# Performance work log

Hardware: AMD Instinct MI355X
Metric: run time of the kernel (lower is better)

Reference implementation:

```python
import jax, jax.numpy as jnp
import numpy as np

B, NN, D = 16, 50, 400
H, DH = 20, 20
ATT_H = 128
NEWS = 20000
K = 10
STEPS, SLOTS = 6, 10
EPS = 1e-5


def _layer_norm(x, g, b):
    m = jnp.mean(x, -1, keepdims=True)
    v = jnp.mean(jnp.square(x - m), -1, keepdims=True)
    return (x - m) * jax.lax.rsqrt(v + EPS) * g + b


def setup_inputs():
    key = jax.random.key(0)
    ks = jax.random.split(key, 9)
    s = 1.0 / np.sqrt(D)
    return {
        "news_input": jax.random.normal(ks[0], (B, NN, D), jnp.float32),
        "outputs_table": jax.random.normal(ks[1], (NEWS, K, D), jnp.float32) * 0.1,
        "Wq": jax.random.normal(ks[2], (D, H * DH), jnp.float32) * s,
        "Wk": jax.random.normal(ks[3], (D, H * DH), jnp.float32) * s,
        "Wv": jax.random.normal(ks[4], (D, H * DH), jnp.float32) * s,
        "ln1_g": jnp.ones((D,), jnp.float32),
        "ln1_b": jnp.zeros((D,), jnp.float32),
        "fc1_w": jax.random.normal(ks[5], (D, ATT_H), jnp.float32) * s,
        "fc1_b": jnp.zeros((ATT_H,), jnp.float32),
        "fc2_w": jax.random.normal(ks[6], (ATT_H, 1), jnp.float32) * (1.0 / np.sqrt(ATT_H)),
        "fc2_b": jnp.zeros((1,), jnp.float32),
        "ln2_g": jnp.ones((D,), jnp.float32),
        "ln2_b": jnp.zeros((D,), jnp.float32),
        "click_history": jax.random.randint(ks[7], (B, NN), 1, NEWS + 1),
        "neighbor_table": jax.random.randint(ks[8], (NEWS + 1, K), 1, NEWS + 1),
        "mask": jnp.ones((B, 50 * SLOTS), jnp.int32),
    }


def _traverse(news_input, outputs_table, click_history, neighbor_table):
    # Vectorized form of the per-item 6-hop neighbor traversal.
    def step(carry, _):
        idx, dead = carry                                          # [B,N] int, [B,N] bool
        vg = outputs_table[idx - 1]                                # [B,N,K,D] gather
        scores = jnp.einsum('bnkd,bnd->bnk', vg, news_input)      # [B,N,K]
        mx_i = jnp.argmax(scores, -1)
        mx_v = jnp.take_along_axis(scores, mx_i[..., None], -1)[..., 0]
        nz = scores != 0
        any_nz = jnp.any(nz, -1)
        nz_i = jnp.argmax(jnp.where(nz, scores, -jnp.inf), -1)
        hop = (mx_v == 0) & jnp.logical_not(dead)                  # max score exactly 0 -> follow graph
        sel_i = jnp.where(hop & any_nz, nz_i, mx_i)
        new_dead = dead | (hop & jnp.logical_not(any_nz))
        nbr = jnp.take_along_axis(neighbor_table[idx], sel_i[..., None], -1)[..., 0]
        new_idx = jnp.where(hop & any_nz, nbr, idx)
        sel = jnp.take_along_axis(vg, sel_i[..., None, None], 2)[..., 0, :]
        sel = jnp.where(new_dead[..., None], 0.0, sel)
        return (new_idx, new_dead), sel

    init = (click_history, jnp.zeros(click_history.shape, bool))
    _, sels = jax.lax.scan(step, init, None, length=STEPS)         # [6,B,N,D]
    sels = jnp.moveaxis(sels, 0, 2)                                # [B,N,6,D]
    valid = jnp.any(news_input != 0, -1).astype(sels.dtype)        # skip all-zero news rows
    sels = sels * valid[..., None, None]
    res = jnp.pad(sels, ((0, 0), (0, 0), (0, SLOTS - STEPS), (0, 0)))
    if NN < 50:
        res = jnp.pad(res, ((0, 0), (0, 50 - NN), (0, 0), (0, 0)))
    return res                                                      # [B,50,10,D]


def _mha(x, mask, Wq, Wk, Wv):
    L = x.shape[1]
    q = (x @ Wq).reshape(-1, L, H, DH).transpose(0, 2, 1, 3)
    k = (x @ Wk).reshape(-1, L, H, DH).transpose(0, 2, 1, 3)
    v = (x @ Wv).reshape(-1, L, H, DH).transpose(0, 2, 1, 3)
    sc = jnp.einsum('bhqd,bhkd->bhqk', q, k) / np.float32(np.sqrt(DH))
    sc = jnp.where(mask[:, None, None, :] > 0, sc, -1e9)
    a = jax.nn.softmax(sc, -1)
    o = jnp.einsum('bhqk,bhkd->bhqd', a, v)
    return o.transpose(0, 2, 1, 3).reshape(-1, L, H * DH)


def _att_pool(x, mask, fc1_w, fc1_b, fc2_w, fc2_b):
    e = jnp.tanh(x @ fc1_w + fc1_b) @ fc2_w + fc2_b                # [B*50,10,1]
    e = jnp.where(mask[..., None] > 0, e, -1e9)
    a = jax.nn.softmax(e, 1)
    return jnp.sum(a * x, 1)


def reference(news_input, outputs_table, Wq, Wk, Wv, ln1_g, ln1_b,
              fc1_w, fc1_b, fc2_w, fc2_b, ln2_g, ln2_b,
              click_history, neighbor_table, mask):
    res = _traverse(news_input, outputs_table, click_history, neighbor_table)
    x = res.reshape(-1, 50 * SLOTS, D)
    x = _mha(x, mask, Wq, Wk, Wv)
    x = x.reshape(-1, SLOTS, D)
    x = _layer_norm(x, ln1_g, ln1_b)
    x = _att_pool(x, mask.reshape(-1, SLOTS), fc1_w, fc1_b, fc2_w, fc2_b)
    x = _layer_norm(x, ln2_g, ln2_b)
    return x.reshape(-1, 50, D)
```

## Files before the change

### kernel.cpp

```cpp
#include <hip/hip_runtime.h>
#include <hip/hip_bf16.h>
#include <math.h>

#define B 16
#define NN 50
#define D 400
#define H 20
#define DH 20
#define ATT_H 128
#define NEWS 20000
#define K 10
#define STEPS 6
#define SLOTS 10
#define L 500
#define EPS 1e-5f

#define XP 416
#define NC 1200

typedef short short8 __attribute__((ext_vector_type(8)));
typedef float floatx4 __attribute__((ext_vector_type(4)));

__device__ __forceinline__ short f2bf(float f) {
    __hip_bfloat16 h = __float2bfloat16(f);
    return *reinterpret_cast<short*>(&h);
}

__global__ __launch_bounds__(256) void k_traverse(
    const float* __restrict__ news,
    const float* __restrict__ table,
    const int*   __restrict__ click,
    const int*   __restrict__ nbrt,
    short* __restrict__ x)
{
    __shared__ float ssc[K];

    int item = blockIdx.x;
    int b = item / NN, n = item % NN;
    int tid = threadIdx.x;
    int lane = tid & 63, w = tid >> 6;

    float nv[7];
    bool nzf = false;
    #pragma unroll
    for (int i = 0; i < 7; i++) {
        int d = lane + 64 * i;
        float v = (d < D) ? news[(size_t)item * D + d] : 0.0f;
        nv[i] = v;
        nzf |= (v != 0.0f);
    }
    float valid = __any(nzf) ? 1.0f : 0.0f;

    int idx = click[item];
    bool dead = false;
    short* xbase = x + (size_t)(b * L + n * SLOTS) * XP;

    for (int step = 0; step < STEPS; step++) {
        const float* tb = table + (size_t)(idx - 1) * K * D;
        for (int kk = w; kk < K; kk += 4) {
            float p = 0.0f;
            #pragma unroll
            for (int i = 0; i < 7; i++) {
                int d = lane + 64 * i;
                if (d < D) p += tb[kk * D + d] * nv[i];
            }
            #pragma unroll
            for (int off = 32; off > 0; off >>= 1) p += __shfl_xor(p, off);
            if (lane == 0) ssc[kk] = p;
        }
        __syncthreads();

        float scores[K];
        #pragma unroll
        for (int kk = 0; kk < K; kk++) scores[kk] = ssc[kk];

        int mx_i = 0; float mx_v = scores[0];
        #pragma unroll
        for (int kk = 1; kk < K; kk++)
            if (scores[kk] > mx_v) { mx_v = scores[kk]; mx_i = kk; }

        bool any_nz = false; int nz_i = 0; float nz_v = -INFINITY;
        #pragma unroll
        for (int kk = 0; kk < K; kk++) {
            if (scores[kk] != 0.0f) {
                if (!any_nz || scores[kk] > nz_v) { nz_v = scores[kk]; nz_i = kk; }
                any_nz = true;
            }
        }

        bool hop = (mx_v == 0.0f) && !dead;
        int sel_i = (hop && any_nz) ? nz_i : mx_i;
        bool new_dead = dead || (hop && !any_nz);
        int nbr = nbrt[(size_t)idx * K + sel_i];
        int new_idx = (hop && any_nz) ? nbr : idx;

        float scale = new_dead ? 0.0f : valid;
        const float* selrow = tb + (size_t)sel_i * D;
        short* xr = xbase + (size_t)step * XP;
        for (int d = tid; d < XP; d += 256)
            xr[d] = (d < D) ? f2bf(selrow[d] * scale) : (short)0;

        idx = new_idx; dead = new_dead;
        __syncthreads();
    }
    for (int s = STEPS; s < SLOTS; s++) {
        short* xr = xbase + (size_t)s * XP;
        for (int d = tid; d < XP; d += 256) xr[d] = 0;
    }
}

__global__ __launch_bounds__(256) void k_wconvT(
    const float* __restrict__ Wq, const float* __restrict__ Wk,
    const float* __restrict__ Wv, short* __restrict__ wT)
{
    int c = blockIdx.x;
    int z = c / 400, n = c % 400;
    const float* W = (z == 0) ? Wq : (z == 1) ? Wk : Wv;
    for (int k = threadIdx.x; k < XP; k += 256)
        wT[(size_t)c * XP + k] = (k < 400) ? f2bf(W[(size_t)k * 400 + n]) : (short)0;
}

#define BM 128
#define BN 64
#define BKK 32

__global__ __launch_bounds__(256) void k_qkv_mfma(
    const short* __restrict__ xg,
    const short* __restrict__ wT,
    float* __restrict__ c)
{
    __shared__ short xs[BM][BKK + 8];
    __shared__ short wt[BN][BKK + 8];

    int tid = threadIdx.x;
    int m0 = blockIdx.x * BM;
    int n0 = blockIdx.y * BN;
    int lane = tid & 63, w = tid >> 6;
    int wr = w >> 1, wc = w & 1;
    int quad = lane >> 4, l16 = lane & 15;

    floatx4 acc[4][2];
    #pragma unroll
    for (int i = 0; i < 4; i++)
        #pragma unroll
        for (int j = 0; j < 2; j++) acc[i][j] = (floatx4){0.f, 0.f, 0.f, 0.f};

    int xr = tid >> 1, xc = (tid & 1) * 16;
    int wrow = tid >> 2, wcol8 = (tid & 3) * 8;
    bool xok = (m0 + xr) < 8000;
    bool wok = (n0 + wrow) < NC;

    for (int k0 = 0; k0 < XP; k0 += BKK) {
        int4 xv0 = {0,0,0,0}, xv1 = {0,0,0,0}, wv = {0,0,0,0};
        if (xok) {
            const int4* src = (const int4*)(xg + (size_t)(m0 + xr) * XP + k0 + xc);
            xv0 = src[0]; xv1 = src[1];
        }
        if (wok)
            wv = *(const int4*)(wT + (size_t)(n0 + wrow) * XP + k0 + wcol8);
        __syncthreads();
        *(int4*)&xs[xr][xc]      = xv0;
        *(int4*)&xs[xr][xc + 8]  = xv1;
        *(int4*)&wt[wrow][wcol8] = wv;
        __syncthreads();

        short8 a[4], bf[2];
        #pragma unroll
        for (int fi = 0; fi < 4; fi++)
            a[fi] = *(const short8*)&xs[wr * 64 + fi * 16 + l16][quad * 8];
        #pragma unroll
        for (int fj = 0; fj < 2; fj++)
            bf[fj] = *(const short8*)&wt[wc * 32 + fj * 16 + l16][quad * 8];
        #pragma unroll
        for (int fi = 0; fi < 4; fi++)
            #pragma unroll
            for (int fj = 0; fj < 2; fj++)
                acc[fi][fj] = __builtin_amdgcn_mfma_f32_16x16x32_bf16(
                    a[fi], bf[fj], acc[fi][fj], 0, 0, 0);
    }

    #pragma unroll
    for (int fi = 0; fi < 4; fi++) {
        int grow_base = m0 + wr * 64 + fi * 16 + quad * 4;
        #pragma unroll
        for (int fj = 0; fj < 2; fj++) {
            int gcol = n0 + wc * 32 + fj * 16 + l16;
            #pragma unroll
            for (int r = 0; r < 4; r++) {
                int grow = grow_base + r;
                if (grow < 8000 && gcol < NC)
                    c[(size_t)grow * NC + gcol] = acc[fi][fj][r];
            }
        }
    }
}

#define KSTR 24
#define VSTR 520

__global__ __launch_bounds__(256) void k_attn3(
    const float* __restrict__ qkv,
    const int* __restrict__ mask,
    float* __restrict__ o)
{
    __shared__ short sh[12288 + 32 * VSTR];
    short* VTb = sh + 12288;
    short* Pb  = VTb + 20 * VSTR;
    float* msk = (float*)(Pb + 4 * 16 * 40);

    int b = blockIdx.x / H, h = blockIdx.x % H;
    int tid = threadIdx.x;
    int lane = tid & 63, w = tid >> 6;
    int quad = lane >> 4, l16 = lane & 15;
    const float scale = 0.22360679774997896f;

    for (int i = tid; i < 512 * KSTR; i += 256) {
        int j = i / KSTR, d = i % KSTR;
        float v = (j < L && d < DH) ? qkv[(size_t)(b * L + j) * NC + 400 + h * DH + d] : 0.0f;
        sh[i] = f2bf(v);
    }
    for (int i = tid; i < L * DH; i += 256) {
        int j = i / DH, d = i % DH;
        VTb[d * VSTR + j] = f2bf(qkv[(size_t)(b * L + j) * NC + 800 + h * DH + d]);
    }
    for (int i = tid; i < DH * 12; i += 256) {
        int d = i / 12, j = L + i % 12;
        VTb[d * VSTR + j] = 0;
    }
    for (int i = tid; i < 512; i += 256)
        msk[i] = (i < L && mask[(size_t)b * L + i] > 0) ? 1.0f : 0.0f;
    __syncthreads();

    short* Pw = Pb + w * 16 * 40;

    for (int qt = w; qt < 32; qt += 4) {
        int qrow = qt * 16 + l16;
        const float* qp = qkv + (size_t)(b * L + (qrow < L ? qrow : 0)) * NC + h * DH;
        short8 aq;
        #pragma unroll
        for (int jj = 0; jj < 8; jj++) {
            int k = quad * 8 + jj;
            float v = (qrow < L && k < DH) ? qp[k] * scale : 0.0f;
            aq[jj] = f2bf(v);
        }

        floatx4 O0 = (floatx4){0.f,0.f,0.f,0.f};
        floatx4 O1 = (floatx4){0.f,0.f,0.f,0.f};
        float mrun[4], lrun[4];
        #pragma unroll
        for (int r = 0; r < 4; r++) { mrun[r] = -INFINITY; lrun[r] = 0.0f; }

        for (int jt = 0; jt < 16; jt++) {
            short8 bk0 = (short8)(short)0, bk1 = (short8)(short)0;
            if (quad < 3) {
                bk0 = *(const short8*)&sh[(jt * 32 + l16) * KSTR + quad * 8];
                bk1 = *(const short8*)&sh[(jt * 32 + 16 + l16) * KSTR + quad * 8];
            }
            floatx4 z = (floatx4){0.f,0.f,0.f,0.f};
            floatx4 s0 = __builtin_amdgcn_mfma_f32_16x16x32_bf16(aq, bk0, z, 0, 0, 0);
            floatx4 s1 = __builtin_amdgcn_mfma_f32_16x16x32_bf16(aq, bk1, z, 0, 0, 0);

            float mk0 = msk[jt * 32 + l16];
            float mk1 = msk[jt * 32 + 16 + l16];
            #pragma unroll
            for (int r = 0; r < 4; r++) {
                s0[r] = (mk0 != 0.0f) ? s0[r] : -1e9f;
                s1[r] = (mk1 != 0.0f) ? s1[r] : -1e9f;
            }

            float rmax[4];
            #pragma unroll
            for (int r = 0; r < 4; r++) rmax[r] = fmaxf(s0[r], s1[r]);
            #pragma unroll
            for (int st = 1; st < 16; st <<= 1)
                #pragma unroll
                for (int r = 0; r < 4; r++)
                    rmax[r] = fmaxf(rmax[r], __shfl_xor(rmax[r], st));

            float p0[4], p1[4], rsum[4];
            #pragma unroll
            for (int r = 0; r < 4; r++) {
                float mnew = fmaxf(mrun[r], rmax[r]);
                float alpha = __expf(mrun[r] - mnew);
                mrun[r] = mnew;
                lrun[r] *= alpha;
                O0[r] *= alpha; O1[r] *= alpha;
                p0[r] = __expf(s0[r] - mnew);
                p1[r] = __expf(s1[r] - mnew);
                rsum[r] = p0[r] + p1[r];
            }
            #pragma unroll
            for (int st = 1; st < 16; st <<= 1)
                #pragma unroll
                for (int r = 0; r < 4; r++)
                    rsum[r] += __shfl_xor(rsum[r], st);
            #pragma unroll
            for (int r = 0; r < 4; r++) lrun[r] += rsum[r];

            #pragma unroll
            for (int r = 0; r < 4; r++) {
                Pw[(quad * 4 + r) * 40 + l16]      = f2bf(p0[r]);
                Pw[(quad * 4 + r) * 40 + 16 + l16] = f2bf(p1[r]);
            }
            short8 ap  = *(const short8*)&Pw[l16 * 40 + quad * 8];
            short8 bv0 = *(const short8*)&VTb[l16 * VSTR + jt * 32 + quad * 8];
            short8 bv1 = *(const short8*)&VTb[(16 + l16) * VSTR + jt * 32 + quad * 8];
            O0 = __builtin_amdgcn_mfma_f32_16x16x32_bf16(ap, bv0, O0, 0, 0, 0);
            O1 = __builtin_amdgcn_mfma_f32_16x16x32_bf16(ap, bv1, O1, 0, 0, 0);
        }

        #pragma unroll
        for (int r = 0; r < 4; r++) {
            int grow = qt * 16 + quad * 4 + r;
            if (grow < L) {
                float inv = 1.0f / lrun[r];
                float* op = o + (size_t)(b * L + grow) * (H * DH) + h * DH;
                op[l16] = O0[r] * inv;
                if (l16 < DH - 16) op[16 + l16] = O1[r] * inv;
            }
        }
    }
}

__global__ __launch_bounds__(256) void k_pool(
    const float* __restrict__ o,
    const float* __restrict__ ln1g, const float* __restrict__ ln1b,
    const float* __restrict__ fc1w, const float* __restrict__ fc1b,
    const float* __restrict__ fc2w, const float* __restrict__ fc2b,
    const float* __restrict__ ln2g, const float* __restrict__ ln2b,
    const int* __restrict__ mask,
    float* __restrict__ out)
{
    __shared__ float xt[SLOTS][D];
    __shared__ float hv[SLOTS * ATT_H];
    __shared__ float es[SLOTS];
    __shared__ float red[8];

    int g = blockIdx.x;
    int tid = threadIdx.x;
    int lane = tid & 63, w = tid >> 6;

    const float* xg = o + (size_t)g * SLOTS * D;

    for (int s = w; s < SLOTS; s += 4) {
        const float* xr = xg + (size_t)s * D;
        float vbuf[7];
        float sum = 0.0f, sq = 0.0f;
        #pragma unroll
        for (int i = 0; i < 7; i++) {
            int d = lane + 64 * i;
            float v = (d < D) ? xr[d] : 0.0f;
            vbuf[i] = v; sum += v; sq += v * v;
        }
        #pragma unroll
        for (int off = 32; off > 0; off >>= 1) {
            sum += __shfl_xor(sum, off);
            sq  += __shfl_xor(sq, off);
        }
        float mean = sum / (float)D;
        float var = sq / (float)D - mean * mean;
        float rs = rsqrtf(var + EPS);
        #pragma unroll
        for (int i = 0; i < 7; i++) {
            int d = lane + 64 * i;
            if (d < D) xt[s][d] = (vbuf[i] - mean) * rs * ln1g[d] + ln1b[d];
        }
    }
    __syncthreads();

    {
        int jh = tid & 127;
        int s0 = tid >> 7;
        float hs[5];
        #pragma unroll
        for (int jj = 0; jj < 5; jj++) hs[jj] = fc1b[jh];
        for (int d = 0; d < D; d++) {
            float fw = fc1w[(size_t)d * ATT_H + jh];
            #pragma unroll
            for (int jj = 0; jj < 5; jj++) hs[jj] += xt[s0 + 2 * jj][d] * fw;
        }
        float f2 = fc2w[jh];
        #pragma unroll
        for (int jj = 0; jj < 5; jj++)
            hv[(s0 + 2 * jj) * ATT_H + jh] = tanhf(hs[jj]) * f2;
    }
    __syncthreads();

    for (int s = w; s < SLOTS; s += 4) {
        float p = hv[s * ATT_H + lane] + hv[s * ATT_H + lane + 64];
        #pragma unroll
        for (int off = 32; off > 0; off >>= 1) p += __shfl_xor(p, off);
        if (lane == 0) es[s] = p + fc2b[0];
    }
    __syncthreads();

    float ev[SLOTS];
    float emax = -INFINITY;
    #pragma unroll
    for (int s = 0; s < SLOTS; s++) {
        float e = (mask[(size_t)g * SLOTS + s] > 0) ? es[s] : -1e9f;
        ev[s] = e;
        if (e > emax) emax = e;
    }
    float esum = 0.0f;
    #pragma unroll
    for (int s = 0; s < SLOTS; s++) { ev[s] = __expf(ev[s] - emax); esum += ev[s]; }
    float einv = 1.0f / esum;

    int d0 = tid, d1 = tid + 256;
    float p0 = 0.0f, p1 = 0.0f;
    #pragma unroll
    for (int s = 0; s < SLOTS; s++) {
        p0 += ev[s] * xt[s][d0];
        if (d1 < D) p1 += ev[s] * xt[s][d1];
    }
    p0 *= einv; p1 *= einv;

    float sum = p0 + ((d1 < D) ? p1 : 0.0f);
    float sq  = p0 * p0 + ((d1 < D) ? p1 * p1 : 0.0f);
    #pragma unroll
    for (int off = 32; off > 0; off >>= 1) {
        sum += __shfl_xor(sum, off);
        sq  += __shfl_xor(sq, off);
    }
    if (lane == 0) { red[w] = sum; red[4 + w] = sq; }
    __syncthreads();
    float tsum = red[0] + red[1] + red[2] + red[3];
    float tsq  = red[4] + red[5] + red[6] + red[7];
    float mean = tsum / (float)D;
    float var = tsq / (float)D - mean * mean;
    float rs = rsqrtf(var + EPS);

    float* og = out + (size_t)g * D;
    og[d0] = (p0 - mean) * rs * ln2g[d0] + ln2b[d0];
    if (d1 < D) og[d1] = (p1 - mean) * rs * ln2g[d1] + ln2b[d1];
}

extern "C" void kernel_launch(void* const* d_in, const int* in_sizes, int n_in,
                              void* d_out, int out_size, void* d_ws, size_t ws_size,
                              hipStream_t stream) {
    const float* news  = (const float*)d_in[0];
    const float* table = (const float*)d_in[1];
    const float* Wq    = (const float*)d_in[2];
    const float* Wk    = (const float*)d_in[3];
    const float* Wv    = (const float*)d_in[4];
    const float* ln1g  = (const float*)d_in[5];
    const float* ln1b  = (const float*)d_in[6];
    const float* fc1w  = (const float*)d_in[7];
    const float* fc1b  = (const float*)d_in[8];
    const float* fc2w  = (const float*)d_in[9];
    const float* fc2b  = (const float*)d_in[10];
    const float* ln2g  = (const float*)d_in[11];
    const float* ln2b  = (const float*)d_in[12];
    const int* click   = (const int*)d_in[13];
    const int* nbrt    = (const int*)d_in[14];
    const int* mask    = (const int*)d_in[15];
    float* out = (float*)d_out;

    char* p = (char*)d_ws;
    short* xbf = (short*)p;  p += (size_t)8000 * XP * sizeof(short);
    short* wT  = (short*)p;  p += (size_t)NC * XP * sizeof(short);
    float* qkv = (float*)p;  p += (size_t)8000 * NC * sizeof(float);
    float* ob  = (float*)p;

    k_traverse<<<dim3(B * NN), dim3(256), 0, stream>>>(news, table, click, nbrt, xbf);
    k_wconvT<<<dim3(NC), dim3(256), 0, stream>>>(Wq, Wk, Wv, wT);
    k_qkv_mfma<<<dim3((8000 + BM - 1) / BM, (NC + BN - 1) / BN), dim3(256), 0, stream>>>(
        xbf, wT, qkv);
    k_attn3<<<dim3(B * H), dim3(256), 0, stream>>>(qkv, mask, ob);
    k_pool<<<dim3(B * NN), dim3(256), 0, stream>>>(ob, ln1g, ln1b, fc1w, fc1b, fc2w, fc2b,
                                                   ln2g, ln2b, mask, out);
}
```

Baseline: 622.8 us.

## Split attention queries across blocks and transpose MFMA to cut row reductions

The attention kernel now launches four blocks per (batch, head), each handling a quarter of the query tiles, to raise occupancy. The MFMA operands are swapped so each lane holds one query column. This turns the row max into two cross-quad shuffles, and the softmax denominator is computed by adding a row of ones to V (row 20). Rescaling of the running output is skipped when no lane's max increases, and the mask is stored as bf16. The cost is that each of the four blocks reloads the full K and V tiles for its head.

```diff
diff --git a/kernel.cpp b/kernel.cpp
--- a/kernel.cpp
+++ b/kernel.cpp
@@ -18,6 +18,7 @@
 #define XP 416
 #define NC 1200
 
+typedef short short4v __attribute__((ext_vector_type(4)));
 typedef short short8 __attribute__((ext_vector_type(8)));
 typedef float floatx4 __attribute__((ext_vector_type(4)));
 
@@ -197,18 +198,22 @@
 
 #define KSTR 24
 #define VSTR 520
-
-__global__ __launch_bounds__(256) void k_attn3(
+#define PSTR 40
+#define QSPLIT 4
+
+__global__ __launch_bounds__(256) void k_attn4(
     const float* __restrict__ qkv,
     const int* __restrict__ mask,
     float* __restrict__ o)
 {
-    __shared__ short sh[12288 + 32 * VSTR];
+    __shared__ short sh[12288 + 21 * VSTR + 4 * 16 * PSTR + 512];
     short* VTb = sh + 12288;
-    short* Pb  = VTb + 20 * VSTR;
-    float* msk = (float*)(Pb + 4 * 16 * 40);
-
-    int b = blockIdx.x / H, h = blockIdx.x % H;
+    short* Pb  = VTb + 21 * VSTR;
+    short* msk = Pb + 4 * 16 * PSTR;
+
+    int part = blockIdx.x & (QSPLIT - 1);
+    int bh = blockIdx.x >> 2;
+    int b = bh / H, h = bh % H;
     int tid = threadIdx.x;
     int lane = tid & 63, w = tid >> 6;
     int quad = lane >> 4, l16 = lane & 15;
@@ -223,100 +228,100 @@
         int j = i / DH, d = i % DH;
         VTb[d * VSTR + j] = f2bf(qkv[(size_t)(b * L + j) * NC + 800 + h * DH + d]);
     }
+    for (int j = tid; j < 512; j += 256) {
+        VTb[20 * VSTR + j] = (j < L) ? f2bf(1.0f) : (short)0;
+        msk[j] = (j < L && mask[(size_t)b * L + j] > 0) ? f2bf(1.0f) : (short)0;
+    }
     for (int i = tid; i < DH * 12; i += 256) {
         int d = i / 12, j = L + i % 12;
         VTb[d * VSTR + j] = 0;
     }
-    for (int i = tid; i < 512; i += 256)
-        msk[i] = (i < L && mask[(size_t)b * L + i] > 0) ? 1.0f : 0.0f;
     __syncthreads();
 
-    short* Pw = Pb + w * 16 * 40;
-
-    for (int qt = w; qt < 32; qt += 4) {
+    short* Pw = Pb + w * 16 * PSTR;
+    short* pwr = Pw + l16 * PSTR;
+    const short* prd = Pw + l16 * PSTR + quad * 8;
+    const short* kA  = sh + quad * 8;
+    const short* vA0 = VTb + l16 * VSTR;
+    int r1 = 16 + l16; if (r1 > 20) r1 = 20;
+    const short* vA1 = VTb + r1 * VSTR;
+
+    for (int qt = part * 8 + w; qt < part * 8 + 8; qt += 4) {
         int qrow = qt * 16 + l16;
         const float* qp = qkv + (size_t)(b * L + (qrow < L ? qrow : 0)) * NC + h * DH;
         short8 aq;
         #pragma unroll
         for (int jj = 0; jj < 8; jj++) {
             int k = quad * 8 + jj;
-            float v = (qrow < L && k < DH) ? qp[k] * scale : 0.0f;
+            float v = (k < DH) ? qp[k] * scale : 0.0f;
             aq[jj] = f2bf(v);
         }
 
         floatx4 O0 = (floatx4){0.f,0.f,0.f,0.f};
         floatx4 O1 = (floatx4){0.f,0.f,0.f,0.f};
-        float mrun[4], lrun[4];
-        #pragma unroll
-        for (int r = 0; r < 4; r++) { mrun[r] = -INFINITY; lrun[r] = 0.0f; }
+        float mrun = -INFINITY;
 
         for (int jt = 0; jt < 16; jt++) {
-            short8 bk0 = (short8)(short)0, bk1 = (short8)(short)0;
+            short8 ak0 = (short8)(short)0, ak1 = (short8)(short)0;
             if (quad < 3) {
-                bk0 = *(const short8*)&sh[(jt * 32 + l16) * KSTR + quad * 8];
-                bk1 = *(const short8*)&sh[(jt * 32 + 16 + l16) * KSTR + quad * 8];
+                ak0 = *(const short8*)&kA[(jt * 32 + l16) * KSTR];
+                ak1 = *(const short8*)&kA[(jt * 32 + 16 + l16) * KSTR];
             }
             floatx4 z = (floatx4){0.f,0.f,0.f,0.f};
-            floatx4 s0 = __builtin_amdgcn_mfma_f32_16x16x32_bf16(aq, bk0, z, 0, 0, 0);
-            floatx4 s1 = __builtin_amdgcn_mfma_f32_16x16x32_bf16(aq, bk1, z, 0, 0, 0);
-
-            float mk0 = msk[jt * 32 + l16];
-            float mk1 = msk[jt * 32 + 16 + l16];
+            floatx4 s0 = __builtin_amdgcn_mfma_f32_16x16x32_bf16(ak0, aq, z, 0, 0, 0);
+            floatx4 s1 = __builtin_amdgcn_mfma_f32_16x16x32_bf16(ak1, aq, z, 0, 0, 0);
+
+            short4v mk0 = *(const short4v*)&msk[jt * 32 + quad * 4];
+            short4v mk1 = *(const short4v*)&msk[jt * 32 + 16 + quad * 4];
             #pragma unroll
             for (int r = 0; r < 4; r++) {
-                s0[r] = (mk0 != 0.0f) ? s0[r] : -1e9f;
-                s1[r] = (mk1 != 0.0f) ? s1[r] : -1e9f;
-            }
-
-            float rmax[4];
-            #pragma unroll
-            for (int r = 0; r < 4; r++) rmax[r] = fmaxf(s0[r], s1[r]);
-            #pragma unroll
-            for (int st = 1; st < 16; st <<= 1)
+                s0[r] = (mk0[r] != 0) ? s0[r] : -1e9f;
+                s1[r] = (mk1[r] != 0) ? s1[r] : -1e9f;
+            }
+
+            float mt = fmaxf(fmaxf(fmaxf(s0[0], s0[1]), fmaxf(s0[2], s0[3])),
+                             fmaxf(fmaxf(s1[0], s1[1]), fmaxf(s1[2], s1[3])));
+            mt = fmaxf(mt, __shfl_xor(mt, 16));
+            mt = fmaxf(mt, __shfl_xor(mt, 32));
+
+            if (!__all(mt <= mrun)) {
+                float mnew = fmaxf(mrun, mt);
+                float alpha = __expf(mrun - mnew);
+                mrun = mnew;
                 #pragma unroll
-                for (int r = 0; r < 4; r++)
-                    rmax[r] = fmaxf(rmax[r], __shfl_xor(rmax[r], st));
-
-            float p0[4], p1[4], rsum[4];
+                for (int r = 0; r < 4; r++) { O0[r] *= alpha; O1[r] *= alpha; }
+            }
+
+            short4v pk0, pk1;
             #pragma unroll
             for (int r = 0; r < 4; r++) {
-                float mnew = fmaxf(mrun[r], rmax[r]);
-                float alpha = __expf(mrun[r] - mnew);
-                mrun[r] = mnew;
-                lrun[r] *= alpha;
-                O0[r] *= alpha; O1[r] *= alpha;
-                p0[r] = __expf(s0[r] - mnew);
-                p1[r] = __expf(s1[r] - mnew);
-                rsum[r] = p0[r] + p1[r];
-            }
-            #pragma unroll
-            for (int st = 1; st < 16; st <<= 1)
+                pk0[r] = f2bf(__expf(s0[r] - mrun));
+                pk1[r] = f2bf(__expf(s1[r] - mrun));
+            }
+            *(short4v*)&pwr[quad * 4]      = pk0;
+            *(short4v*)&pwr[16 + quad * 4] = pk1;
+
+            short8 ap  = *(const short8*)prd;
+            short8 va0 = *(const short8*)&vA0[jt * 32 + quad * 8];
+            short8 va1 = *(const short8*)&vA1[jt * 32 + quad * 8];
+            O0 = __builtin_amdgcn_mfma_f32_16x16x32_bf16(va0, ap, O0, 0, 0, 0);
+            O1 = __builtin_amdgcn_mfma_f32_16x16x32_bf16(va1, ap, O1, 0, 0, 0);
+        }
+
+        float lsum = __shfl(O1[0], 16 + l16);
+        float inv = 1.0f / lsum;
+        int q = qt * 16 + l16;
+        if (q < L) {
+            float* op = o + (size_t)(b * L + q) * (H * DH) + h * DH;
+            floatx4 v0;
+            #pragma unroll
+            for (int r = 0; r < 4; r++) v0[r] = O0[r] * inv;
+            *(floatx4*)&op[quad * 4] = v0;
+            if (quad == 0) {
+                floatx4 v1;
                 #pragma unroll
-                for (int r = 0; r < 4; r++)
-                    rsum[r] += __shfl_xor(rsum[r], st);
-            #pragma unroll
-            for (int r = 0; r < 4; r++) lrun[r] += rsum[r];
-
-            #pragma unroll
-            for (int r = 0; r < 4; r++) {
-                Pw[(quad * 4 + r) * 40 + l16]      = f2bf(p0[r]);
-                Pw[(quad * 4 + r) * 40 + 16 + l16] = f2bf(p1[r]);
-            }
-            short8 ap  = *(const short8*)&Pw[l16 * 40 + quad * 8];
-            short8 bv0 = *(const short8*)&VTb[l16 * VSTR + jt * 32 + quad * 8];
-            short8 bv1 = *(const short8*)&VTb[(16 + l16) * VSTR + jt * 32 + quad * 8];
-            O0 = __builtin_amdgcn_mfma_f32_16x16x32_bf16(ap, bv0, O0, 0, 0, 0);
-            O1 = __builtin_amdgcn_mfma_f32_16x16x32_bf16(ap, bv1, O1, 0, 0, 0);
-        }
-
-        #pragma unroll
-        for (int r = 0; r < 4; r++) {
-            int grow = qt * 16 + quad * 4 + r;
-            if (grow < L) {
-                float inv = 1.0f / lrun[r];
-                float* op = o + (size_t)(b * L + grow) * (H * DH) + h * DH;
-                op[l16] = O0[r] * inv;
-                if (l16 < DH - 16) op[16 + l16] = O1[r] * inv;
+                for (int r = 0; r < 4; r++) v1[r] = O1[r] * inv;
+                *(floatx4*)&op[16] = v1;
             }
         }
     }
@@ -467,7 +472,7 @@
     k_wconvT<<<dim3(NC), dim3(256), 0, stream>>>(Wq, Wk, Wv, wT);
     k_qkv_mfma<<<dim3((8000 + BM - 1) / BM, (NC + BN - 1) / BN), dim3(256), 0, stream>>>(
         xbf, wT, qkv);
-    k_attn3<<<dim3(B * H), dim3(256), 0, stream>>>(qkv, mask, ob);
+    k_attn4<<<dim3(B * H * QSPLIT), dim3(256), 0, stream>>>(qkv, mask, ob);
     k_pool<<<dim3(B * NN), dim3(256), 0, stream>>>(ob, ln1g, ln1b, fc1w, fc1b, fc2w, fc2b,
                                                    ln2g, ln2b, mask, out);
 }
```

Result: faster. 551.4 us (-11.5%).
